# Optimization experiments

Hardware: AMD Instinct MI355X
Metric: run time of the kernel (lower is better)

The kernel has to match this reference:

```python
import jax, jax.numpy as jnp
import numpy as np

VOCAB = 8192
BETA = 0.25


def setup_inputs() -> dict:
    key = jax.random.key(0)
    k1, k2 = jax.random.split(key)
    x = jax.random.normal(k1, (16, 1024, 256), dtype=jnp.float32)
    emb = jax.random.normal(k2, (256, VOCAB), dtype=jnp.float32) * 0.05  # xavier-ish scale
    return {"x": x, "emb": emb}


def reference(x, emb):
    C = x.shape[-1]
    x_flat = x.reshape(-1, C)  # [M, C]
    M = x_flat.shape[0]
    distances = ((x_flat ** 2).sum(axis=1, keepdims=True)
                 - 2.0 * jnp.einsum('mc,ck->mk', x_flat, emb)
                 + (emb ** 2).sum(axis=0, keepdims=True))
    # argmax(-d) == argmin(d), same first-occurrence tie-break
    encoding_indices = jnp.argmin(distances, axis=-1)  # [M]
    # direct gather instead of one-hot @ emb (same math)
    quantized = jnp.take(emb, encoding_indices, axis=1).T  # [M, C]
    quantized = quantized.reshape(x.shape)
    e_latent_loss = ((jax.lax.stop_gradient(quantized) - x) ** 2).mean()
    q_latent_loss = ((quantized - jax.lax.stop_gradient(x)) ** 2).mean()
    loss_vq = q_latent_loss + BETA * e_latent_loss
    quantized = x + jax.lax.stop_gradient(quantized - x)  # straight-through
    # avg_probs == one_hot(indices).mean(0) -> normalized histogram
    counts = jnp.zeros((VOCAB,), dtype=x.dtype).at[encoding_indices].add(1.0)
    avg_probs = counts / M
    perplexity = jnp.exp(-jnp.sum(avg_probs * jnp.log(avg_probs + 1e-10)))
    return quantized, loss_vq, perplexity
```

## Files before the change

### kernel.cpp

```cpp
#include <hip/hip_runtime.h>
#include <cfloat>
#include <cmath>

#define VOCAB 8192
#define MTOT 16384
#define CDIM 256
#define KSPLIT 8
#define TAU 0.1f
#define IDX_INF 0x7fffffff

typedef __attribute__((ext_vector_type(8))) short bf16x8;
typedef __attribute__((ext_vector_type(4))) float f32x4;

#define AS1 __attribute__((address_space(1)))
#define AS3 __attribute__((address_space(3)))

__device__ __forceinline__ void gl_lds16(const void* g, void* l) {
  __builtin_amdgcn_global_load_lds((const AS1 unsigned int*)g,
                                   (AS3 unsigned int*)l, 16, 0, 0);
}

__device__ inline ushort f2bf(float f) {
  unsigned u = __float_as_uint(f);
  unsigned r = (u + 0x7fffu + ((u >> 16) & 1u)) >> 16;
  return (ushort)r;
}

__global__ void vq_enorm_kernel(const float* __restrict__ emb,
                                float* __restrict__ enorm,
                                double* __restrict__ enormd) {
  __shared__ double sd[4][64];
  int tid = threadIdx.x;
  int kk = tid & 63, cg = tid >> 6;
  int k = blockIdx.x * 64 + kk;
  double s = 0.0;
  for (int c = cg * 64; c < cg * 64 + 64; ++c) {
    float v = emb[(size_t)c * VOCAB + k];
    s += (double)v * (double)v;
  }
  sd[cg][kk] = s;
  __syncthreads();
  if (cg == 0) {
    double t = sd[0][kk] + sd[1][kk] + sd[2][kk] + sd[3][kk];
    enorm[k] = (float)t;
    enormd[k] = t;
  }
}

__global__ void vq_prep_embT_kernel(const float* __restrict__ emb,
                                    float* __restrict__ embT) {
  __shared__ float t[32][33];
  int bc = blockIdx.x & 7;
  int bk = blockIdx.x >> 3;
  int lx = threadIdx.x & 31, lyq = threadIdx.x >> 5;
#pragma unroll
  for (int yy = 0; yy < 4; ++yy) {
    int y = lyq * 4 + yy;
    t[y][lx] = emb[(size_t)(bc * 32 + y) * VOCAB + bk * 32 + lx];
  }
  __syncthreads();
#pragma unroll
  for (int yy = 0; yy < 4; ++yy) {
    int y = lyq * 4 + yy;
    embT[(size_t)(bk * 32 + y) * CDIM + bc * 32 + lx] = t[lx][y];
  }
}

__global__ void vq_pack_x_kernel(const float* __restrict__ x,
                                 ushort* __restrict__ xb) {
  int u = blockIdx.x * 256 + threadIdx.x;
  int rb = u >> 12;
  int o = u & 4095;
  int cc = o >> 9, w = o & 511;
  int pair = w >> 3, sswz = w & 7;
  int s = sswz ^ (pair & 7);
  int row = pair * 2 + (s >> 2);
  int g = s & 3;
  const float* src = x + (size_t)(rb * 128 + row) * CDIM + cc * 32 + g * 8;
  float4 v0 = *(const float4*)src;
  float4 v1 = *(const float4*)(src + 4);
  float a[8] = {v0.x, v0.y, v0.z, v0.w, v1.x, v1.y, v1.z, v1.w};
  bf16x8 h;
#pragma unroll
  for (int j = 0; j < 8; ++j) h[j] = (short)f2bf(-2.0f * a[j]);
  *(bf16x8*)(xb + (size_t)u * 8) = h;
}

__global__ void vq_pack_e_kernel(const float* __restrict__ embT,
                                 ushort* __restrict__ eb) {
  int u = blockIdx.x * 256 + threadIdx.x;
  int sp = u >> 15;
  int r = u & 32767;
  int ct = (r >> 14) & 1, chunk = (r >> 11) & 7;
  int o16 = r & 2047;
  int wcg = o16 >> 9, w = o16 & 511;
  int pair = w >> 3, sswz = w & 7;
  int s = sswz ^ (pair & 7);
  int cloc = pair * 2 + (s >> 2);
  int g = s & 3;
  int code = sp * 1024 + ct * 512 + wcg * 128 + cloc;
  int dims = chunk * 32 + g * 8;
  const float* src = embT + (size_t)code * CDIM + dims;
  float4 v0 = *(const float4*)src;
  float4 v1 = *(const float4*)(src + 4);
  float a[8] = {v0.x, v0.y, v0.z, v0.w, v1.x, v1.y, v1.z, v1.w};
  bf16x8 h;
#pragma unroll
  for (int j = 0; j < 8; ++j) h[j] = (short)f2bf(a[j]);
  *(bf16x8*)(eb + (size_t)u * 8) = h;
}

__global__ __launch_bounds__(512, 2) void vq_dist_kernel(
    const ushort* __restrict__ xb, const ushort* __restrict__ eb,
    const float* __restrict__ enorm,
    float4* __restrict__ pkd, int4* __restrict__ pki) {
  __shared__ ushort Abuf[32768];
  __shared__ ushort Bbuf[2][16384];

  const int tid = threadIdx.x;
  const int lane = tid & 63, wid = tid >> 6;
  const int wr = wid >> 2, wc = wid & 3;
  const int l15 = lane & 15, lg = lane >> 4;
  const int rb = blockIdx.x >> 3, sp = blockIdx.x & 7;
  const int m0 = rb * 128;
  const int spbase = sp * 1024;

  {
    const ushort* xs = xb + (size_t)rb * 32768;
#pragma unroll
    for (int i = 0; i < 8; ++i)
      gl_lds16(xs + (wid * 8 + i) * 512 + lane * 8, &Abuf[(wid * 8 + i) * 512]);
    const ushort* bs = eb + (size_t)sp * 262144;
#pragma unroll
    for (int i = 0; i < 4; ++i)
      gl_lds16(bs + (wid * 4 + i) * 512 + lane * 8, &Bbuf[0][(wid * 4 + i) * 512]);
  }

  uint offA[4], offB[8];
#pragma unroll
  for (int mf = 0; mf < 4; ++mf) {
    int row = wr * 64 + mf * 16 + l15;
    int pr = row >> 1, s = ((row & 1) << 2) | lg;
    offA[mf] = pr * 128 + ((s ^ (pr & 7)) << 4);
  }
#pragma unroll
  for (int nf = 0; nf < 8; ++nf) {
    int cl = nf * 16 + l15;
    int pr = cl >> 1, s = ((cl & 1) << 2) | lg;
    offB[nf] = wc * 8192 + pr * 128 + ((s ^ (pr & 7)) << 4);
  }

  float bv[16];
  int bi[16];
#pragma unroll
  for (int s = 0; s < 16; ++s) { bv[s] = FLT_MAX; bi[s] = IDX_INF; }

#pragma unroll
  for (int ct = 0; ct < 2; ++ct) {
    float e16[8];
#pragma unroll
    for (int nf = 0; nf < 8; ++nf)
      e16[nf] = enorm[spbase + ct * 512 + wc * 128 + nf * 16 + l15];
    f32x4 acc[4][8];
#pragma unroll
    for (int mf = 0; mf < 4; ++mf)
#pragma unroll
      for (int nf = 0; nf < 8; ++nf)
        acc[mf][nf] = (f32x4){e16[nf], e16[nf], e16[nf], e16[nf]};

#pragma unroll
    for (int cc = 0; cc < 8; ++cc) {
      const int step = ct * 8 + cc;
      __syncthreads();
      if (step < 15) {
        const ushort* bs = eb + (size_t)sp * 262144 + (size_t)(step + 1) * 16384;
        ushort* dst = &Bbuf[(step + 1) & 1][0];
#pragma unroll
        for (int i = 0; i < 4; ++i)
          gl_lds16(bs + (wid * 4 + i) * 512 + lane * 8, dst + (wid * 4 + i) * 512);
      }
      const char* Ab = (const char*)Abuf + cc * 8192;
      const char* Bb = (const char*)&Bbuf[cc & 1][0];
      bf16x8 af[4];
#pragma unroll
      for (int mf = 0; mf < 4; ++mf) af[mf] = *(const bf16x8*)(Ab + offA[mf]);
#pragma unroll
      for (int nf = 0; nf < 8; ++nf) {
        bf16x8 bfr = *(const bf16x8*)(Bb + offB[nf]);
#pragma unroll
        for (int mf = 0; mf < 4; ++mf)
          acc[mf][nf] = __builtin_amdgcn_mfma_f32_16x16x32_bf16(af[mf], bfr, acc[mf][nf], 0, 0, 0);
      }
    }
#pragma unroll
    for (int nf = 0; nf < 8; ++nf) {
      int n = spbase + ct * 512 + wc * 128 + nf * 16 + l15;
#pragma unroll
      for (int mf = 0; mf < 4; ++mf)
#pragma unroll
        for (int r = 0; r < 4; ++r) {
          float d = acc[mf][nf][r];
          int s = mf * 4 + r;
          if (d < bv[s]) { bv[s] = d; bi[s] = n; }
        }
    }
  }

  __syncthreads();
  float* kd = (float*)Abuf;
  int* ki = (int*)Abuf + 8192;
#pragma unroll
  for (int mf = 0; mf < 4; ++mf)
#pragma unroll
    for (int r = 0; r < 4; ++r) {
      int row = wr * 64 + mf * 16 + lg * 4 + r;
      int idx = (wc * 128 + row) * 16 + l15;
      kd[idx] = bv[mf * 4 + r];
      ki[idx] = bi[mf * 4 + r];
    }
  __syncthreads();
  float* kod = (float*)&Bbuf[0][0];
  int* koi = (int*)&Bbuf[0][0] + 1024;
  {
    int row = tid >> 2, part = tid & 3;
    const float* rd = kd + (part * 128 + row) * 16;
    const int* ri = ki + (part * 128 + row) * 16;
    float d0 = FLT_MAX, d1 = FLT_MAX;
    int i0 = IDX_INF, i1 = IDX_INF;
#pragma unroll
    for (int j = 0; j < 16; ++j) {
      float a = rd[j];
      int ai = ri[j];
      if (a < d0 || (a == d0 && ai < i0)) { d1 = d0; i1 = i0; d0 = a; i0 = ai; }
      else if (a < d1 || (a == d1 && ai < i1)) { d1 = a; i1 = ai; }
    }
    int o = (row * 4 + part) * 2;
    kod[o] = d0; kod[o + 1] = d1;
    koi[o] = i0; koi[o + 1] = i1;
  }
  __syncthreads();
  if (tid < 128) {
    const float* rd = kod + tid * 8;
    const int* ri = koi + tid * 8;
    float d[4] = {FLT_MAX, FLT_MAX, FLT_MAX, FLT_MAX};
    int ix[4] = {IDX_INF, IDX_INF, IDX_INF, IDX_INF};
#pragma unroll
    for (int j = 0; j < 8; ++j) {
      float a = rd[j];
      int ai = ri[j];
#pragma unroll
      for (int q = 0; q < 4; ++q) {
        bool lt = (a < d[q]) || (a == d[q] && ai < ix[q]);
        float td = lt ? d[q] : a;
        int ti = lt ? ix[q] : ai;
        d[q] = lt ? a : d[q];
        ix[q] = lt ? ai : ix[q];
        a = td; ai = ti;
      }
    }
    pkd[(size_t)sp * MTOT + m0 + tid] = make_float4(d[0], d[1], d[2], d[3]);
    pki[(size_t)sp * MTOT + m0 + tid] = make_int4(ix[0], ix[1], ix[2], ix[3]);
  }
}

__global__ void vq_gather_kernel(
    const float* __restrict__ x, const float* __restrict__ embT,
    const double* __restrict__ enormd,
    const float4* __restrict__ pkd, const int4* __restrict__ pki,
    float* __restrict__ out, int* __restrict__ counts, float* __restrict__ ssep) {
  const int wid = threadIdx.x >> 6, lane = threadIdx.x & 63;
  const int m = blockIdx.x * 4 + wid;

  const float4 xq = *(const float4*)(x + (size_t)m * CDIM + lane * 4);

  float bd = FLT_MAX, sd = FLT_MAX;
  int bidx = IDX_INF;
#pragma unroll
  for (int sp2 = 0; sp2 < KSPLIT; ++sp2) {
    float4 dv = pkd[(size_t)sp2 * MTOT + m];
    int4 iv = pki[(size_t)sp2 * MTOT + m];
    float ds[4] = {dv.x, dv.y, dv.z, dv.w};
    int is[4] = {iv.x, iv.y, iv.z, iv.w};
#pragma unroll
    for (int j = 0; j < 4; ++j) {
      float dj = ds[j];
      int ij = is[j];
      if (dj < bd || (dj == bd && ij < bidx)) { sd = bd; bd = dj; bidx = ij; }
      else sd = fminf(sd, dj);
    }
  }
  int best = bidx;
  if (sd - bd < TAU) {
    double bD = DBL_MAX;
    int bn = IDX_INF;
    for (int sp2 = 0; sp2 < KSPLIT; ++sp2) {
      int4 iv = pki[(size_t)sp2 * MTOT + m];
      int is[4] = {iv.x, iv.y, iv.z, iv.w};
#pragma unroll
      for (int j = 0; j < 4; ++j) {
        int cj = is[j];
        const float4 ev = *(const float4*)(embT + (size_t)cj * CDIM + lane * 4);
        double p = (double)xq.x * ev.x + (double)xq.y * ev.y
                 + (double)xq.z * ev.z + (double)xq.w * ev.w;
#pragma unroll
        for (int off = 1; off < 64; off <<= 1) p += __shfl_xor(p, off, 64);
        double dj = enormd[cj] - 2.0 * p;
        if (dj < bD || (dj == bD && cj < bn)) { bD = dj; bn = cj; }
      }
    }
    best = bn;
  }
  const float4 ev = *(const float4*)(embT + (size_t)best * CDIM + lane * 4);
  *(float4*)(out + (size_t)m * CDIM + lane * 4) = ev;
  float dx = ev.x - xq.x, dy = ev.y - xq.y, dz = ev.z - xq.z, dw = ev.w - xq.w;
  float v = dx * dx + dy * dy + dz * dz + dw * dw;
#pragma unroll
  for (int off = 32; off > 0; off >>= 1) v += __shfl_down(v, off, 64);
  if (lane == 0) {
    ssep[m] = v;
    atomicAdd(&counts[best], 1);
  }
}

__global__ void vq_final1_kernel(const float* __restrict__ ssep,
                                 const int* __restrict__ counts,
                                 double* __restrict__ part) {
  __shared__ double red[256];
  const int tid = threadIdx.x, b = blockIdx.x;
  red[tid] = (double)ssep[b * 256 + tid];
  __syncthreads();
  for (int off = 128; off > 0; off >>= 1) {
    if (tid < off) red[tid] += red[tid + off];
    __syncthreads();
  }
  if (tid == 0) part[b] = red[0];
  __syncthreads();
  double e = 0.0;
  if (tid < 128) {
    double p = (double)counts[b * 128 + tid] / (double)MTOT;
    e = p * log(p + 1e-10);
  }
  red[tid] = e;
  __syncthreads();
  for (int off = 128; off > 0; off >>= 1) {
    if (tid < off) red[tid] += red[tid + off];
    __syncthreads();
  }
  if (tid == 0) part[64 + b] = red[0];
}

__global__ void vq_final2_kernel(const double* __restrict__ part,
                                 float* __restrict__ out) {
  const int lane = threadIdx.x;
  double s = part[lane], e = part[64 + lane];
#pragma unroll
  for (int off = 32; off > 0; off >>= 1) {
    s += __shfl_down(s, off, 64);
    e += __shfl_down(e, off, 64);
  }
  if (lane == 0) {
    out[(size_t)MTOT * CDIM] = (float)(1.25 * s / (double)((size_t)MTOT * CDIM));
    out[(size_t)MTOT * CDIM + 1] = (float)exp(-e);
  }
}

extern "C" void kernel_launch(void* const* d_in, const int* in_sizes, int n_in,
                              void* d_out, int out_size, void* d_ws, size_t ws_size,
                              hipStream_t stream) {
  const float* x = (const float*)d_in[0];
  const float* emb = (const float*)d_in[1];
  float* out = (float*)d_out;
  char* ws = (char*)d_ws;

  double* enormd = (double*)(ws);
  float* enorm   = (float*)(ws + 65536);
  float4* pkd    = (float4*)(ws + 98304);
  int4* pki      = (int4*)(ws + 2195456);
  int* counts    = (int*)(ws + 4292608);
  float* ssep    = (float*)(ws + 4325376);
  double* part   = (double*)(ws + 4390912);
  float* embT    = (float*)(ws + 4391936);
  ushort* xb     = (ushort*)(ws + 12780544);
  ushort* eb     = (ushort*)(ws + 21169152);

  hipMemsetAsync(counts, 0, VOCAB * sizeof(int), stream);
  vq_enorm_kernel<<<VOCAB / 64, 256, 0, stream>>>(emb, enorm, enormd);
  vq_prep_embT_kernel<<<(VOCAB / 32) * (CDIM / 32), 256, 0, stream>>>(emb, embT);
  vq_pack_e_kernel<<<(VOCAB * CDIM / 8) / 256, 256, 0, stream>>>(embT, eb);
  vq_pack_x_kernel<<<(MTOT * CDIM / 8) / 256, 256, 0, stream>>>(x, xb);
  vq_dist_kernel<<<(MTOT / 128) * KSPLIT, 512, 0, stream>>>(xb, eb, enorm, pkd, pki);
  vq_gather_kernel<<<MTOT / 4, 256, 0, stream>>>(x, embT, enormd, pkd, pki,
                                                 out, counts, ssep);
  vq_final1_kernel<<<64, 256, 0, stream>>>(ssep, counts, part);
  vq_final2_kernel<<<1, 64, 0, stream>>>(part, out);
}
```

Before: 191.8 us.

## Restructure distance GEMM into per-wave private B streams with shuffle-based top-2 reduction

The distance kernel now uses 64-row blocks of 256 threads. Each wave owns a private 256-code slice of the codebook and streams it through its own double-buffered LDS area, so block-wide __syncthreads are replaced by waitcnt fences. The pack kernels are re-laid-out to match the new smaller tiles and swizzle. The per-row top-4 candidate reduction now does a cross-lane top-2 shuffle merge before one small LDS pass, replacing the two-stage LDS reduction. This aims to cut barrier stalls and LDS traffic, but it halves A-tile reuse per block, doubles grid size, and re-reads each x tile for every wave.

```diff
diff --git a/kernel.cpp b/kernel.cpp
--- a/kernel.cpp
+++ b/kernel.cpp
@@ -24,6 +24,17 @@
   unsigned u = __float_as_uint(f);
   unsigned r = (u + 0x7fffu + ((u >> 16) & 1u)) >> 16;
   return (ushort)r;
+}
+
+__device__ inline void top2_merge(float& b, int& i, float& s, int& si,
+                                  float ob, int oi, float os, int osi) {
+  if (ob < b || (ob == b && oi < i)) {
+    if (b < os || (b == os && i < osi)) { s = b; si = i; }
+    else { s = os; si = osi; }
+    b = ob; i = oi;
+  } else {
+    if (ob < s || (ob == s && oi < si)) { s = ob; si = oi; }
+  }
 }
 
 __global__ void vq_enorm_kernel(const float* __restrict__ emb,
@@ -69,14 +80,9 @@
 __global__ void vq_pack_x_kernel(const float* __restrict__ x,
                                  ushort* __restrict__ xb) {
   int u = blockIdx.x * 256 + threadIdx.x;
-  int rb = u >> 12;
-  int o = u & 4095;
-  int cc = o >> 9, w = o & 511;
-  int pair = w >> 3, sswz = w & 7;
-  int s = sswz ^ (pair & 7);
-  int row = pair * 2 + (s >> 2);
-  int g = s & 3;
-  const float* src = x + (size_t)(rb * 128 + row) * CDIM + cc * 32 + g * 8;
+  int slot = u & 3, row = (u >> 2) & 63, cc = (u >> 8) & 7, rb = u >> 11;
+  int dims = cc * 32 + ((slot ^ (row & 3)) << 3);
+  const float* src = x + (size_t)(rb * 64 + row) * CDIM + dims;
   float4 v0 = *(const float4*)src;
   float4 v1 = *(const float4*)(src + 4);
   float a[8] = {v0.x, v0.y, v0.z, v0.w, v1.x, v1.y, v1.z, v1.w};
@@ -89,18 +95,11 @@
 __global__ void vq_pack_e_kernel(const float* __restrict__ embT,
                                  ushort* __restrict__ eb) {
   int u = blockIdx.x * 256 + threadIdx.x;
-  int sp = u >> 15;
-  int r = u & 32767;
-  int ct = (r >> 14) & 1, chunk = (r >> 11) & 7;
-  int o16 = r & 2047;
-  int wcg = o16 >> 9, w = o16 & 511;
-  int pair = w >> 3, sswz = w & 7;
-  int s = sswz ^ (pair & 7);
-  int cloc = pair * 2 + (s >> 2);
-  int g = s & 3;
-  int code = sp * 1024 + ct * 512 + wcg * 128 + cloc;
-  int dims = chunk * 32 + g * 8;
-  const float* src = embT + (size_t)code * CDIM + dims;
+  int slot = u & 3, code = (u >> 2) & 63, cc = (u >> 8) & 7;
+  int cg = (u >> 11) & 3, wcp = (u >> 13) & 3, sp = u >> 15;
+  int cglob = sp * 1024 + wcp * 256 + cg * 64 + code;
+  int dims = cc * 32 + ((slot ^ (code & 3)) << 3);
+  const float* src = embT + (size_t)cglob * CDIM + dims;
   float4 v0 = *(const float4*)src;
   float4 v1 = *(const float4*)(src + 4);
   float a[8] = {v0.x, v0.y, v0.z, v0.w, v1.x, v1.y, v1.z, v1.w};
@@ -110,91 +109,100 @@
   *(bf16x8*)(eb + (size_t)u * 8) = h;
 }
 
-__global__ __launch_bounds__(512, 2) void vq_dist_kernel(
+__global__ __launch_bounds__(256, 2) void vq_dist_kernel(
     const ushort* __restrict__ xb, const ushort* __restrict__ eb,
     const float* __restrict__ enorm,
     float4* __restrict__ pkd, int4* __restrict__ pki) {
-  __shared__ ushort Abuf[32768];
-  __shared__ ushort Bbuf[2][16384];
+  __shared__ ushort Abuf[16384];
+  __shared__ ushort Bbuf[4][2][2048];
+  __shared__ float msd[2][4][64];
+  __shared__ int msi[2][4][64];
 
   const int tid = threadIdx.x;
-  const int lane = tid & 63, wid = tid >> 6;
-  const int wr = wid >> 2, wc = wid & 3;
+  const int lane = tid & 63, wc = tid >> 6;
   const int l15 = lane & 15, lg = lane >> 4;
   const int rb = blockIdx.x >> 3, sp = blockIdx.x & 7;
-  const int m0 = rb * 128;
-  const int spbase = sp * 1024;
-
-  {
-    const ushort* xs = xb + (size_t)rb * 32768;
-#pragma unroll
-    for (int i = 0; i < 8; ++i)
-      gl_lds16(xs + (wid * 8 + i) * 512 + lane * 8, &Abuf[(wid * 8 + i) * 512]);
-    const ushort* bs = eb + (size_t)sp * 262144;
-#pragma unroll
-    for (int i = 0; i < 4; ++i)
-      gl_lds16(bs + (wid * 4 + i) * 512 + lane * 8, &Bbuf[0][(wid * 4 + i) * 512]);
-  }
-
-  uint offA[4], offB[8];
+  const int m0 = rb * 64;
+  const int nbase = sp * 1024 + wc * 256;
+
+  const ushort* xs = xb + (size_t)rb * 16384;
+  const ushort* ebw = eb + (size_t)(sp * 4 + wc) * 65536;
+
+#pragma unroll
+  for (int i = 0; i < 8; ++i)
+    gl_lds16(xs + (wc * 8 + i) * 512 + lane * 8, &Abuf[(wc * 8 + i) * 512]);
+#pragma unroll
+  for (int i = 0; i < 4; ++i)
+    gl_lds16(ebw + i * 512 + lane * 8, &Bbuf[wc][0][i * 512]);
+
+  float en[16];
+#pragma unroll
+  for (int cg = 0; cg < 4; ++cg)
+#pragma unroll
+    for (int nf = 0; nf < 4; ++nf)
+      en[cg * 4 + nf] = enorm[nbase + cg * 64 + nf * 16 + l15];
+
+  __syncthreads();
+
+  uint offA[4], offB[4];
 #pragma unroll
   for (int mf = 0; mf < 4; ++mf) {
-    int row = wr * 64 + mf * 16 + l15;
-    int pr = row >> 1, s = ((row & 1) << 2) | lg;
-    offA[mf] = pr * 128 + ((s ^ (pr & 7)) << 4);
-  }
-#pragma unroll
-  for (int nf = 0; nf < 8; ++nf) {
-    int cl = nf * 16 + l15;
-    int pr = cl >> 1, s = ((cl & 1) << 2) | lg;
-    offB[nf] = wc * 8192 + pr * 128 + ((s ^ (pr & 7)) << 4);
-  }
+    int row = mf * 16 + l15;
+    offA[mf] = row * 64 + ((lg ^ (row & 3)) << 4);
+  }
+#pragma unroll
+  for (int nf = 0; nf < 4; ++nf) {
+    int code = nf * 16 + l15;
+    offB[nf] = code * 64 + ((lg ^ (code & 3)) << 4);
+  }
+  const char* Bbase = (const char*)&Bbuf[wc][0][0];
 
   float bv[16];
   int bi[16];
 #pragma unroll
-  for (int s = 0; s < 16; ++s) { bv[s] = FLT_MAX; bi[s] = IDX_INF; }
-
-#pragma unroll
-  for (int ct = 0; ct < 2; ++ct) {
-    float e16[8];
-#pragma unroll
-    for (int nf = 0; nf < 8; ++nf)
-      e16[nf] = enorm[spbase + ct * 512 + wc * 128 + nf * 16 + l15];
-    f32x4 acc[4][8];
+  for (int s = 0; s < 16; ++s) { bv[s] = FLT_MAX; bi[s] = 0; }
+
+#pragma unroll
+  for (int cg = 0; cg < 4; ++cg) {
+    f32x4 acc[4][4];
 #pragma unroll
     for (int mf = 0; mf < 4; ++mf)
 #pragma unroll
-      for (int nf = 0; nf < 8; ++nf)
-        acc[mf][nf] = (f32x4){e16[nf], e16[nf], e16[nf], e16[nf]};
-
+      for (int nf = 0; nf < 4; ++nf) {
+        float e = en[cg * 4 + nf];
+        acc[mf][nf] = (f32x4){e, e, e, e};
+      }
 #pragma unroll
     for (int cc = 0; cc < 8; ++cc) {
-      const int step = ct * 8 + cc;
-      __syncthreads();
-      if (step < 15) {
-        const ushort* bs = eb + (size_t)sp * 262144 + (size_t)(step + 1) * 16384;
-        ushort* dst = &Bbuf[(step + 1) & 1][0];
+      const int t = cg * 8 + cc;
+      asm volatile("s_waitcnt lgkmcnt(0)" ::: "memory");
+      if (t < 31) {
+        const ushort* src = ebw + (size_t)(t + 1) * 2048;
+        char* dst = (char*)&Bbuf[wc][(t + 1) & 1][0];
 #pragma unroll
         for (int i = 0; i < 4; ++i)
-          gl_lds16(bs + (wid * 4 + i) * 512 + lane * 8, dst + (wid * 4 + i) * 512);
-      }
-      const char* Ab = (const char*)Abuf + cc * 8192;
-      const char* Bb = (const char*)&Bbuf[cc & 1][0];
-      bf16x8 af[4];
+          gl_lds16(src + i * 512 + lane * 8, dst + i * 1024);
+        asm volatile("s_waitcnt vmcnt(4)" ::: "memory");
+      } else {
+        asm volatile("s_waitcnt vmcnt(0)" ::: "memory");
+      }
+      __builtin_amdgcn_sched_barrier(0);
+      const char* Ab = (const char*)Abuf + cc * 4096;
+      const char* Bb = Bbase + (cc & 1) * 4096;
+      bf16x8 af[4], bfr[4];
 #pragma unroll
       for (int mf = 0; mf < 4; ++mf) af[mf] = *(const bf16x8*)(Ab + offA[mf]);
 #pragma unroll
-      for (int nf = 0; nf < 8; ++nf) {
-        bf16x8 bfr = *(const bf16x8*)(Bb + offB[nf]);
-#pragma unroll
-        for (int mf = 0; mf < 4; ++mf)
-          acc[mf][nf] = __builtin_amdgcn_mfma_f32_16x16x32_bf16(af[mf], bfr, acc[mf][nf], 0, 0, 0);
-      }
-    }
-#pragma unroll
-    for (int nf = 0; nf < 8; ++nf) {
-      int n = spbase + ct * 512 + wc * 128 + nf * 16 + l15;
+      for (int nf = 0; nf < 4; ++nf) bfr[nf] = *(const bf16x8*)(Bb + offB[nf]);
+#pragma unroll
+      for (int mf = 0; mf < 4; ++mf)
+#pragma unroll
+        for (int nf = 0; nf < 4; ++nf)
+          acc[mf][nf] = __builtin_amdgcn_mfma_f32_16x16x32_bf16(af[mf], bfr[nf], acc[mf][nf], 0, 0, 0);
+    }
+#pragma unroll
+    for (int nf = 0; nf < 4; ++nf) {
+      int n = nbase + cg * 64 + nf * 16 + l15;
 #pragma unroll
       for (int mf = 0; mf < 4; ++mf)
 #pragma unroll
@@ -206,58 +214,47 @@
     }
   }
 
-  __syncthreads();
-  float* kd = (float*)Abuf;
-  int* ki = (int*)Abuf + 8192;
 #pragma unroll
   for (int mf = 0; mf < 4; ++mf)
 #pragma unroll
     for (int r = 0; r < 4; ++r) {
-      int row = wr * 64 + mf * 16 + lg * 4 + r;
-      int idx = (wc * 128 + row) * 16 + l15;
-      kd[idx] = bv[mf * 4 + r];
-      ki[idx] = bi[mf * 4 + r];
-    }
-  __syncthreads();
-  float* kod = (float*)&Bbuf[0][0];
-  int* koi = (int*)&Bbuf[0][0] + 1024;
-  {
-    int row = tid >> 2, part = tid & 3;
-    const float* rd = kd + (part * 128 + row) * 16;
-    const int* ri = ki + (part * 128 + row) * 16;
-    float d0 = FLT_MAX, d1 = FLT_MAX;
-    int i0 = IDX_INF, i1 = IDX_INF;
-#pragma unroll
-    for (int j = 0; j < 16; ++j) {
-      float a = rd[j];
-      int ai = ri[j];
-      if (a < d0 || (a == d0 && ai < i0)) { d1 = d0; i1 = i0; d0 = a; i0 = ai; }
-      else if (a < d1 || (a == d1 && ai < i1)) { d1 = a; i1 = ai; }
-    }
-    int o = (row * 4 + part) * 2;
-    kod[o] = d0; kod[o + 1] = d1;
-    koi[o] = i0; koi[o + 1] = i1;
-  }
-  __syncthreads();
-  if (tid < 128) {
-    const float* rd = kod + tid * 8;
-    const int* ri = koi + tid * 8;
+      int s = mf * 4 + r;
+      float b = bv[s], sec = FLT_MAX;
+      int i = bi[s], si = IDX_INF;
+#pragma unroll
+      for (int m = 1; m < 16; m <<= 1) {
+        float ob = __shfl_xor(b, m, 64);
+        float os = __shfl_xor(sec, m, 64);
+        int oi = __shfl_xor(i, m, 64);
+        int osi = __shfl_xor(si, m, 64);
+        top2_merge(b, i, sec, si, ob, oi, os, osi);
+      }
+      if (l15 == 0) {
+        int row = mf * 16 + lg * 4 + r;
+        msd[0][wc][row] = b; msi[0][wc][row] = i;
+        msd[1][wc][row] = sec; msi[1][wc][row] = si;
+      }
+    }
+  __syncthreads();
+  if (tid < 64) {
     float d[4] = {FLT_MAX, FLT_MAX, FLT_MAX, FLT_MAX};
     int ix[4] = {IDX_INF, IDX_INF, IDX_INF, IDX_INF};
 #pragma unroll
-    for (int j = 0; j < 8; ++j) {
-      float a = rd[j];
-      int ai = ri[j];
-#pragma unroll
-      for (int q = 0; q < 4; ++q) {
-        bool lt = (a < d[q]) || (a == d[q] && ai < ix[q]);
-        float td = lt ? d[q] : a;
-        int ti = lt ? ix[q] : ai;
-        d[q] = lt ? a : d[q];
-        ix[q] = lt ? ai : ix[q];
-        a = td; ai = ti;
-      }
-    }
+    for (int w = 0; w < 4; ++w)
+#pragma unroll
+      for (int e = 0; e < 2; ++e) {
+        float a = msd[e][w][tid];
+        int ai = msi[e][w][tid];
+#pragma unroll
+        for (int q = 0; q < 4; ++q) {
+          bool lt = (a < d[q]) || (a == d[q] && ai < ix[q]);
+          float td = lt ? d[q] : a;
+          int ti = lt ? ix[q] : ai;
+          d[q] = lt ? a : d[q];
+          ix[q] = lt ? ai : ix[q];
+          a = td; ai = ti;
+        }
+      }
     pkd[(size_t)sp * MTOT + m0 + tid] = make_float4(d[0], d[1], d[2], d[3]);
     pki[(size_t)sp * MTOT + m0 + tid] = make_int4(ix[0], ix[1], ix[2], ix[3]);
   }
@@ -388,7 +385,7 @@
   vq_prep_embT_kernel<<<(VOCAB / 32) * (CDIM / 32), 256, 0, stream>>>(emb, embT);
   vq_pack_e_kernel<<<(VOCAB * CDIM / 8) / 256, 256, 0, stream>>>(embT, eb);
   vq_pack_x_kernel<<<(MTOT * CDIM / 8) / 256, 256, 0, stream>>>(x, xb);
-  vq_dist_kernel<<<(MTOT / 128) * KSPLIT, 512, 0, stream>>>(xb, eb, enorm, pkd, pki);
+  vq_dist_kernel<<<(MTOT / 64) * KSPLIT, 256, 0, stream>>>(xb, eb, enorm, pkd, pki);
   vq_gather_kernel<<<MTOT / 4, 256, 0, stream>>>(x, embT, enormd, pkd, pki,
                                                  out, counts, ssep);
   vq_final1_kernel<<<64, 256, 0, stream>>>(ssep, counts, part);
```

Result: slower. 269.6 us (+40.6%).
